# Kernel tuning notes

Measured on AMD Instinct MI355X. Metric: run time of the kernel, lower is better.

## Reference

```python
import jax, jax.numpy as jnp
import numpy as np

B, S, E, H = 4, 2048, 1024, 16
D = E // H
LR_MULT = 100.0
EPS = 1e-5

def setup_inputs() -> dict:
    key = jax.random.key(0)
    ks = jax.random.split(key, 4)
    x = jax.random.normal(ks[0], (B, S, E), dtype=jnp.float32)
    # nn.MultiheadAttention in_proj_weight [3E,E], out_proj.weight [E,E] (bias=False)
    W_qkv = jax.random.normal(ks[1], (3 * E, E), dtype=jnp.float32) * (1.0 / np.sqrt(E))
    W_o = jax.random.normal(ks[2], (E, E), dtype=jnp.float32) * (1.0 / np.sqrt(E))
    ln_w = jnp.ones((E,), dtype=jnp.float32)
    scaler = jnp.asarray(1.0 / LR_MULT, dtype=jnp.float32)
    return {"x": x, "W_qkv": W_qkv, "W_o": W_o, "ln_w": ln_w, "scaler": scaler}

def _layernorm(x, w):
    mu = jnp.mean(x, axis=-1, keepdims=True)
    var = jnp.mean(jnp.square(x - mu), axis=-1, keepdims=True)
    return (x - mu) * jax.lax.rsqrt(var + EPS) * w

def reference(x, W_qkv, W_o, ln_w, scaler):
    resid = x
    xn = _layernorm(x, ln_w)
    qkv = jnp.einsum('bse,fe->bsf', xn, W_qkv)  # [B,S,3E]
    q, k, v = jnp.split(qkv, 3, axis=-1)
    q = q.reshape(B, S, H, D)
    k = k.reshape(B, S, H, D)
    v = v.reshape(B, S, H, D)
    scores = jnp.einsum('bihd,bjhd->bhij', q, k) / jnp.sqrt(jnp.asarray(D, x.dtype))
    # linear_encoding_base[i,j] = j - i; bias = softplus(100*scaler)*(j-i) where j<=i else -inf
    i_idx = jnp.arange(S)
    rel = (i_idx[None, :] - i_idx[:, None]).astype(x.dtype)  # j - i
    causal = i_idx[None, :] <= i_idx[:, None]                # tril: j <= i
    slope = jax.nn.softplus(LR_MULT * scaler)
    bias = jnp.where(causal, slope * rel, -jnp.inf)          # [S,S]
    att = jax.nn.softmax(scores + bias[None, None, :, :], axis=-1)
    out = jnp.einsum('bhij,bjhd->bihd', att, v).reshape(B, S, E)
    out = jnp.einsum('bse,fe->bsf', out, W_o)
    return out + resid
```

## Files before the change

kernel.cpp:

```cpp
#include <hip/hip_runtime.h>

typedef unsigned short u16;
typedef unsigned int u32;
typedef __bf16 bf16x8 __attribute__((ext_vector_type(8)));
typedef float f32x4 __attribute__((ext_vector_type(4)));

#define B_ 4
#define S_ 2048
#define E_ 1024
#define H_ 16
#define D_ 64

__device__ __forceinline__ u16 f2bf(float f) {
  u32 u = __float_as_uint(f);
  u32 r = u + 0x7fffu + ((u >> 16) & 1u);
  return (u16)(r >> 16);
}

__device__ __forceinline__ void gload16(const u16* g, u16* l) {
  __builtin_amdgcn_global_load_lds((const __attribute__((address_space(1))) void*)g,
                                   (__attribute__((address_space(3))) void*)l, 16, 0, 0);
}

__global__ __launch_bounds__(256) void prep_kernel(const float* __restrict__ x,
                                                   const float* __restrict__ lnw,
                                                   u16* __restrict__ xn,
                                                   const float* __restrict__ Wqkv,
                                                   u16* __restrict__ wqkvb,
                                                   const float* __restrict__ Wo,
                                                   u16* __restrict__ wob) {
  const int b = blockIdx.x;
  if (b < 2048) {
    const int lane = threadIdx.x & 63;
    const int wv = threadIdx.x >> 6;
    const int row = b * 4 + wv;
    const float4* xr = (const float4*)(x + (size_t)row * E_);
    float4 vv[4];
    float s = 0.f, sq = 0.f;
#pragma unroll
    for (int i = 0; i < 4; ++i) {
      vv[i] = xr[lane + i * 64];
      s += vv[i].x + vv[i].y + vv[i].z + vv[i].w;
      sq += vv[i].x * vv[i].x + vv[i].y * vv[i].y + vv[i].z * vv[i].z + vv[i].w * vv[i].w;
    }
#pragma unroll
    for (int off = 1; off < 64; off <<= 1) {
      s += __shfl_xor(s, off);
      sq += __shfl_xor(sq, off);
    }
    const float mu = s * (1.f / E_);
    const float rs = rsqrtf(sq * (1.f / E_) - mu * mu + 1e-5f);
    u16* xo = xn + (size_t)row * E_;
    const float4* wr = (const float4*)lnw;
#pragma unroll
    for (int i = 0; i < 4; ++i) {
      float4 w4 = wr[lane + i * 64];
      ushort4 o;
      o.x = f2bf((vv[i].x - mu) * rs * w4.x);
      o.y = f2bf((vv[i].y - mu) * rs * w4.y);
      o.z = f2bf((vv[i].z - mu) * rs * w4.z);
      o.w = f2bf((vv[i].w - mu) * rs * w4.w);
      ((ushort4*)xo)[lane + i * 64] = o;
    }
  } else {
    const float* src = (b < 5120) ? Wqkv : Wo;
    u16* dst = (b < 5120) ? wqkvb : wob;
    const int i = (b < 5120 ? b - 2048 : b - 5120) * 256 + threadIdx.x;
    float4 v = ((const float4*)src)[i];
    ushort4 o;
    o.x = f2bf(v.x);
    o.y = f2bf(v.y);
    o.z = f2bf(v.z);
    o.w = f2bf(v.w);
    ((ushort4*)dst)[i] = o;
  }
}

__global__ __launch_bounds__(512, 2) void gemm8_qkv(const u16* __restrict__ A,
                                                    const u16* __restrict__ Bw,
                                                    u16* __restrict__ qo,
                                                    u16* __restrict__ ko,
                                                    u16* __restrict__ vo) {
  constexpr int K = 1024;
  constexpr int NT = K / 64;
  __shared__ u16 lds[2][2][256 * 64];
  const int t = threadIdx.x;
  const int lane = t & 63, wv = t >> 6;
  const int wm = wv >> 2, wn = wv & 3;
  const int m0 = blockIdx.y * 256, n0 = blockIdx.x * 256;
  const int r16 = lane & 15, g4 = lane >> 4;
  const int l3 = lane >> 3, l7 = lane & 7;
  const int colsrc = ((l7 ^ l3) * 8);

  f32x4 acc[8][4] = {};
  bf16x8 af[8][2];
  bf16x8 bfr[2][2];

  auto issue = [&](int ph, int buf, int kt) {
#pragma unroll
    for (int s = 0; s < 2; ++s) {
      const int j = wv * 2 + s;
      int c, m;
      if (ph == 0)      { m = 0; c = j + (j & 8); }
      else if (ph == 1) { m = 1; c = (j >> 2) * 8 + (j & 3); }
      else if (ph == 2) { m = 0; c = 8 + j + (j & 8); }
      else              { m = 1; c = (j >> 2) * 8 + 4 + (j & 3); }
      const u16* src = (m == 0 ? A + (size_t)(m0 + c * 8 + l3) * K
                               : Bw + (size_t)(n0 + c * 8 + l3) * K) + kt + colsrc;
      gload16(src, &lds[buf][m][c * 512]);
    }
  };

  auto loadA = [&](const u16* As, int half) {
#pragma unroll
    for (int i = 0; i < 4; ++i) {
      const int mi = half * 4 + i;
      const int r = wm * 128 + mi * 16 + r16;
      const int sw = (r & 7) << 3;
#pragma unroll
      for (int kc = 0; kc < 2; ++kc)
        af[mi][kc] = *(const bf16x8*)&As[r * 64 + ((kc * 32 + g4 * 8) ^ sw)];
    }
  };
  auto loadB = [&](const u16* Bs, int pair) {
#pragma unroll
    for (int n2 = 0; n2 < 2; ++n2) {
      const int r = wn * 64 + (pair * 2 + n2) * 16 + r16;
      const int sw = (r & 7) << 3;
#pragma unroll
      for (int kc = 0; kc < 2; ++kc)
        bfr[n2][kc] = *(const bf16x8*)&Bs[r * 64 + ((kc * 32 + g4 * 8) ^ sw)];
    }
  };
  auto mmac = [&](int mhalf, int npair) {
#pragma unroll
    for (int i = 0; i < 4; ++i)
#pragma unroll
      for (int n2 = 0; n2 < 2; ++n2)
#pragma unroll
        for (int kc = 0; kc < 2; ++kc)
          acc[mhalf * 4 + i][npair * 2 + n2] = __builtin_amdgcn_mfma_f32_16x16x32_bf16(
              af[mhalf * 4 + i][kc], bfr[n2][kc], acc[mhalf * 4 + i][npair * 2 + n2], 0, 0, 0);
  };

  issue(0, 0, 0);
  issue(1, 0, 0);
  issue(2, 0, 0);
  issue(3, 0, 0);
  asm volatile("s_waitcnt vmcnt(0)" ::: "memory");
  __builtin_amdgcn_s_barrier();

  for (int kt2 = 0; kt2 < NT - 1; ++kt2) {
    const int cur = kt2 & 1;
    const u16* As = lds[cur][0];
    const u16* Bs = lds[cur][1];
    const int ktN = (kt2 + 1) * 64;
    loadA(As, 0);
    loadB(Bs, 0);
    issue(0, cur ^ 1, ktN);
    issue(1, cur ^ 1, ktN);
    issue(2, cur ^ 1, ktN);
    issue(3, cur ^ 1, ktN);
    __builtin_amdgcn_s_barrier();
    asm volatile("s_waitcnt lgkmcnt(0)" ::: "memory");
    asm volatile("s_waitcnt vmcnt(10)" ::: "memory");
    __builtin_amdgcn_sched_barrier(0);
    __builtin_amdgcn_s_setprio(1);
    mmac(0, 0);
    __builtin_amdgcn_s_setprio(0);
    __builtin_amdgcn_s_barrier();
    loadA(As, 1);
    __builtin_amdgcn_s_barrier();
    asm volatile("s_waitcnt lgkmcnt(0)" ::: "memory");
    asm volatile("s_waitcnt vmcnt(8)" ::: "memory");
    __builtin_amdgcn_sched_barrier(0);
    __builtin_amdgcn_s_setprio(1);
    mmac(1, 0);
    __builtin_amdgcn_s_setprio(0);
    __builtin_amdgcn_s_barrier();
    loadB(Bs, 1);
    __builtin_amdgcn_s_barrier();
    asm volatile("s_waitcnt lgkmcnt(0)" ::: "memory");
    asm volatile("s_waitcnt vmcnt(4)" ::: "memory");
    __builtin_amdgcn_sched_barrier(0);
    __builtin_amdgcn_s_setprio(1);
    mmac(1, 1);
    mmac(0, 1);
    __builtin_amdgcn_s_setprio(0);
    __builtin_amdgcn_s_barrier();
  }
  {
    const int cur = (NT - 1) & 1;
    const u16* As = lds[cur][0];
    const u16* Bs = lds[cur][1];
    loadA(As, 0);
    loadB(Bs, 0);
    __builtin_amdgcn_s_barrier();
    asm volatile("s_waitcnt lgkmcnt(0)" ::: "memory");
    asm volatile("s_waitcnt vmcnt(2)" ::: "memory");
    __builtin_amdgcn_sched_barrier(0);
    __builtin_amdgcn_s_setprio(1);
    mmac(0, 0);
    __builtin_amdgcn_s_setprio(0);
    __builtin_amdgcn_s_barrier();
    loadA(As, 1);
    __builtin_amdgcn_s_barrier();
    asm volatile("s_waitcnt lgkmcnt(0)" ::: "memory");
    asm volatile("s_waitcnt vmcnt(0)" ::: "memory");
    __builtin_amdgcn_sched_barrier(0);
    __builtin_amdgcn_s_setprio(1);
    mmac(1, 0);
    __builtin_amdgcn_s_setprio(0);
    __builtin_amdgcn_s_barrier();
    loadB(Bs, 1);
    asm volatile("s_waitcnt lgkmcnt(0)" ::: "memory");
    __builtin_amdgcn_sched_barrier(0);
    __builtin_amdgcn_s_setprio(1);
    mmac(1, 1);
    mmac(0, 1);
    __builtin_amdgcn_s_setprio(0);
  }

  const int which = n0 >> 10;
  u16* dst = which == 0 ? qo : (which == 1 ? ko : vo);
#pragma unroll
  for (int mi = 0; mi < 8; ++mi)
#pragma unroll
    for (int e = 0; e < 4; ++e) {
      const int gr = m0 + wm * 128 + mi * 16 + g4 * 4 + e;
      const int bb = gr >> 11, ss = gr & 2047;
#pragma unroll
      for (int ni = 0; ni < 4; ++ni) {
        const int gc = n0 + wn * 64 + ni * 16 + r16;
        const int hh = (gc >> 6) & 15;
        const int dd = gc & 63;
        dst[(((size_t)bb * H_ + hh) * S_ + ss) * D_ + dd] = f2bf(acc[mi][ni][e]);
      }
    }
}

__global__ __launch_bounds__(256, 2) void gemm_bt1(const u16* __restrict__ A,
                                                   const u16* __restrict__ Bw,
                                                   const int K,
                                                   const float* __restrict__ xres,
                                                   float* __restrict__ outp) {
  __shared__ u16 lds[2][2][128 * 64];
  const int t = threadIdx.x;
  const int lane = t & 63, wv = t >> 6;
  const int wm = wv >> 1, wn = wv & 1;
  const int d = blockIdx.y * 8 + blockIdx.x;
  const int lin = (d & 7) * 64 + (d >> 3);
  const int m0 = (lin & 63) * 128, n0 = (lin >> 6) * 128;
  const int r16 = lane & 15, g4 = lane >> 4;

  const f32x4 fzero = {0.f, 0.f, 0.f, 0.f};
  f32x4 acc[4][4];
#pragma unroll
  for (int i = 0; i < 4; ++i)
#pragma unroll
    for (int j = 0; j < 4; ++j) acc[i][j] = fzero;

  const int srow8 = lane >> 3;
  const int scol = (lane & 7) * 8;

  auto stage = [&](int bu, int kt) {
#pragma unroll
    for (int i = 0; i < 4; ++i) {
      const int c = wv * 4 + i;
      const int row = c * 8 + srow8;
      gload16(A + (size_t)(m0 + row) * K + kt + scol, &lds[bu][0][c * 512]);
      gload16(Bw + (size_t)(n0 + row) * K + kt + scol, &lds[bu][1][c * 512]);
    }
  };

  auto compute = [&](int bu) {
    const u16* As = lds[bu][0];
    const u16* Bs = lds[bu][1];
    bf16x8 af[4][2], bfr[4][2];
#pragma unroll
    for (int mi = 0; mi < 4; ++mi)
#pragma unroll
      for (int kc = 0; kc < 2; ++kc)
        af[mi][kc] = *(const bf16x8*)&As[(wm * 64 + mi * 16 + r16) * 64 + kc * 32 + g4 * 8];
#pragma unroll
    for (int ni = 0; ni < 4; ++ni)
#pragma unroll
      for (int kc = 0; kc < 2; ++kc)
        bfr[ni][kc] = *(const bf16x8*)&Bs[(wn * 64 + ni * 16 + r16) * 64 + kc * 32 + g4 * 8];
#pragma unroll
    for (int mi = 0; mi < 4; ++mi)
#pragma unroll
      for (int ni = 0; ni < 4; ++ni)
#pragma unroll
        for (int kc = 0; kc < 2; ++kc)
          acc[mi][ni] = __builtin_amdgcn_mfma_f32_16x16x32_bf16(af[mi][kc], bfr[ni][kc],
                                                                acc[mi][ni], 0, 0, 0);
  };

  stage(0, 0);
  __syncthreads();
  int cur = 0;
  for (int kt = 64; kt < K; kt += 64) {
    stage(cur ^ 1, kt);
    compute(cur);
    __syncthreads();
    cur ^= 1;
  }
  compute(cur);

#pragma unroll
  for (int mi = 0; mi < 4; ++mi)
#pragma unroll
    for (int e = 0; e < 4; ++e) {
      const int gr = m0 + wm * 64 + mi * 16 + g4 * 4 + e;
#pragma unroll
      for (int ni = 0; ni < 4; ++ni) {
        const int gc = n0 + wn * 64 + ni * 16 + r16;
        const size_t idx = (size_t)gr * 1024 + gc;
        outp[idx] = acc[mi][ni][e] + xres[idx];
      }
    }
}

__global__ __launch_bounds__(256) void attn_kernel(const u16* __restrict__ q,
                                                   const u16* __restrict__ k,
                                                   const u16* __restrict__ v,
                                                   const float* __restrict__ scaler_p,
                                                   u16* __restrict__ ao) {
  __shared__ u16 Qs[64 * 72];
  __shared__ u16 Ks[64 * 72];
  __shared__ u16 Vt[64 * 72];
  __shared__ u16 Ps[4 * 16 * 72];
  const int t = threadIdx.x;
  const int lane = t & 63, wv = t >> 6;
  const int r16 = lane & 15, g4 = lane >> 4;
  const int it = blockIdx.x;
  const int bh = blockIdx.y;
  const int bb = bh >> 4, hh = bh & 15;
  const size_t base = (size_t)bh * (S_ * D_);

  const float tt = 100.f * scaler_p[0];
  const float slope = (tt > 20.f) ? tt : log1pf(expf(tt));
  const float L2E = 1.4426950408889634f;
  const float qs_l2e = 0.125f * L2E;
  const float sl_l2e = slope * L2E;
  int nb = (int)ceilf(80.f / (slope * 64.f));
  if (nb < 1) nb = 1;
  int jt0 = it - nb;
  if (jt0 < 0) jt0 = 0;

  {
    const int r = t >> 2, c = (t & 3) << 4;
    const u16* gp = q + base + (size_t)(it * 64 + r) * D_ + c;
    uint4 a0 = ((const uint4*)gp)[0];
    uint4 a1 = ((const uint4*)gp)[1];
    *(uint4*)&Qs[r * 72 + c] = a0;
    *(uint4*)&Qs[r * 72 + c + 8] = a1;
  }

  float mrun[4] = {-3e38f, -3e38f, -3e38f, -3e38f};
  float lrun[4] = {0.f, 0.f, 0.f, 0.f};
  const f32x4 fzero = {0.f, 0.f, 0.f, 0.f};
  f32x4 oacc[4];
#pragma unroll
  for (int i = 0; i < 4; ++i) oacc[i] = fzero;

  bf16x8 qa[2];
  bool qloaded = false;

  for (int jt = jt0; jt <= it; ++jt) {
    {
      const int r = t >> 2, c = (t & 3) << 4;
      const u16* kg = k + base + (size_t)(jt * 64 + r) * D_ + c;
      uint4 k0 = ((const uint4*)kg)[0];
      uint4 k1 = ((const uint4*)kg)[1];
      *(uint4*)&Ks[r * 72 + c] = k0;
      *(uint4*)&Ks[r * 72 + c + 8] = k1;
      const u16* vg = v + base + (size_t)(jt * 64 + r) * D_ + c;
      union { uint4 u; u16 s[8]; } v0, v1;
      v0.u = ((const uint4*)vg)[0];
      v1.u = ((const uint4*)vg)[1];
#pragma unroll
      for (int j = 0; j < 8; ++j) {
        Vt[(c + j) * 72 + r] = v0.s[j];
        Vt[(c + 8 + j) * 72 + r] = v1.s[j];
      }
    }
    __syncthreads();
    if (!qloaded) {
      qloaded = true;
#pragma unroll
      for (int kc = 0; kc < 2; ++kc)
        qa[kc] = *(const bf16x8*)&Qs[(wv * 16 + r16) * 72 + kc * 32 + g4 * 8];
    }
    f32x4 sfr[4];
#pragma unroll
    for (int nt = 0; nt < 4; ++nt) {
      sfr[nt] = fzero;
#pragma unroll
      for (int kc = 0; kc < 2; ++kc) {
        bf16x8 kb = *(const bf16x8*)&Ks[(nt * 16 + r16) * 72 + kc * 32 + g4 * 8];
        sfr[nt] = __builtin_amdgcn_mfma_f32_16x16x32_bf16(qa[kc], kb, sfr[nt], 0, 0, 0);
      }
    }
    const bool diag = (jt == it);
    const float jb = (float)((jt - it) * 64);
    float pm[4] = {-3e38f, -3e38f, -3e38f, -3e38f};
#pragma unroll
    for (int nt = 0; nt < 4; ++nt) {
      const int jl = nt * 16 + r16;
#pragma unroll
      for (int e = 0; e < 4; ++e) {
        const int il = wv * 16 + g4 * 4 + e;
        float sc = sfr[nt][e] * qs_l2e + sl_l2e * (jb + (float)(jl - il));
        if (diag && jl > il) sc = -3e38f;
        sfr[nt][e] = sc;
        pm[e] = fmaxf(pm[e], sc);
      }
    }
#pragma unroll
    for (int e = 0; e < 4; ++e) {
#pragma unroll
      for (int off = 1; off < 16; off <<= 1) pm[e] = fmaxf(pm[e], __shfl_xor(pm[e], off));
    }
    u16* Psw = Ps + wv * (16 * 72);
    float psum[4] = {0.f, 0.f, 0.f, 0.f};
#pragma unroll
    for (int e = 0; e < 4; ++e) {
      const float mn = fmaxf(mrun[e], pm[e]);
      const float rsc = exp2f(mrun[e] - mn);
      mrun[e] = mn;
      lrun[e] *= rsc;
#pragma unroll
      for (int nt = 0; nt < 4; ++nt) oacc[nt][e] *= rsc;
    }
#pragma unroll
    for (int nt = 0; nt < 4; ++nt)
#pragma unroll
      for (int e = 0; e < 4; ++e) {
        const float p = exp2f(sfr[nt][e] - mrun[e]);
        psum[e] += p;
        Psw[(g4 * 4 + e) * 72 + nt * 16 + r16] = f2bf(p);
      }
#pragma unroll
    for (int e = 0; e < 4; ++e) {
#pragma unroll
      for (int off = 1; off < 16; off <<= 1) psum[e] += __shfl_xor(psum[e], off);
      lrun[e] += psum[e];
    }
    bf16x8 pa[2];
#pragma unroll
    for (int jk = 0; jk < 2; ++jk)
      pa[jk] = *(const bf16x8*)&Psw[r16 * 72 + jk * 32 + g4 * 8];
#pragma unroll
    for (int nt = 0; nt < 4; ++nt)
#pragma unroll
      for (int jk = 0; jk < 2; ++jk) {
        bf16x8 vb = *(const bf16x8*)&Vt[(nt * 16 + r16) * 72 + jk * 32 + g4 * 8];
        oacc[nt] = __builtin_amdgcn_mfma_f32_16x16x32_bf16(pa[jk], vb, oacc[nt], 0, 0, 0);
      }
    __syncthreads();
  }
#pragma unroll
  for (int e = 0; e < 4; ++e) {
    const float inv = 1.f / lrun[e];
    const int row = it * 64 + wv * 16 + g4 * 4 + e;
#pragma unroll
    for (int nt = 0; nt < 4; ++nt) {
      const int col = hh * 64 + nt * 16 + r16;
      ao[((size_t)bb * S_ + row) * E_ + col] = f2bf(oacc[nt][e] * inv);
    }
  }
}

extern "C" void kernel_launch(void* const* d_in, const int* in_sizes, int n_in,
                              void* d_out, int out_size, void* d_ws, size_t ws_size,
                              hipStream_t stream) {
  const float* x = (const float*)d_in[0];
  const float* Wqkv = (const float*)d_in[1];
  const float* Wo = (const float*)d_in[2];
  const float* lnw = (const float*)d_in[3];
  const float* scaler = (const float*)d_in[4];
  float* out = (float*)d_out;
  char* ws = (char*)d_ws;

  u16* xn = (u16*)(ws + 0);
  u16* q = (u16*)(ws + 16777216);
  u16* kk = (u16*)(ws + 33554432);
  u16* vv = (u16*)(ws + 50331648);
  u16* ao = (u16*)(ws + 67108864);
  u16* wqkvb = (u16*)(ws + 83886080);
  u16* wob = (u16*)(ws + 90177536);

  prep_kernel<<<6144, 256, 0, stream>>>(x, lnw, xn, Wqkv, wqkvb, Wo, wob);
  gemm8_qkv<<<dim3(12, 32), 512, 0, stream>>>(xn, wqkvb, q, kk, vv);
  attn_kernel<<<dim3(32, 64), 256, 0, stream>>>(q, kk, vv, scaler, ao);
  gemm_bt1<<<dim3(8, 64), 256, 0, stream>>>(ao, wob, 1024, x, out);
}
```

Before: 139.4 us.

## Single-buffer QKV GEMM LDS with phased in-place refills to raise occupancy

Halves the QKV GEMM's shared memory by replacing the double-buffered LDS tiles with one buffer. Each phase of the next k-tile is loaded in place once the registers have read the data it overwrites. Launch bounds go from 2 to 4 blocks per CU to exploit the freed LDS and hide latency with more resident waves. The cost is a tighter cross-wave dependency, since writes can only start after everyone has finished reading that region. Register pressure may also rise, because the 128-entry accumulator must fit the tighter occupancy bound.

```diff
diff --git a/kernel.cpp b/kernel.cpp
--- a/kernel.cpp
+++ b/kernel.cpp
@@ -76,14 +76,14 @@
   }
 }
 
-__global__ __launch_bounds__(512, 2) void gemm8_qkv(const u16* __restrict__ A,
+__global__ __launch_bounds__(512, 4) void gemm8_qkv(const u16* __restrict__ A,
                                                     const u16* __restrict__ Bw,
                                                     u16* __restrict__ qo,
                                                     u16* __restrict__ ko,
                                                     u16* __restrict__ vo) {
   constexpr int K = 1024;
   constexpr int NT = K / 64;
-  __shared__ u16 lds[2][2][256 * 64];
+  __shared__ u16 lds[2][256 * 64];
   const int t = threadIdx.x;
   const int lane = t & 63, wv = t >> 6;
   const int wm = wv >> 2, wn = wv & 3;
@@ -96,7 +96,7 @@
   bf16x8 af[8][2];
   bf16x8 bfr[2][2];
 
-  auto issue = [&](int ph, int buf, int kt) {
+  auto issue = [&](int ph, int kt) {
 #pragma unroll
     for (int s = 0; s < 2; ++s) {
       const int j = wv * 2 + s;
@@ -107,11 +107,12 @@
       else              { m = 1; c = (j >> 2) * 8 + 4 + (j & 3); }
       const u16* src = (m == 0 ? A + (size_t)(m0 + c * 8 + l3) * K
                                : Bw + (size_t)(n0 + c * 8 + l3) * K) + kt + colsrc;
-      gload16(src, &lds[buf][m][c * 512]);
-    }
-  };
-
-  auto loadA = [&](const u16* As, int half) {
+      gload16(src, &lds[m][c * 512]);
+    }
+  };
+
+  auto loadA = [&](int half) {
+    const u16* As = lds[0];
 #pragma unroll
     for (int i = 0; i < 4; ++i) {
       const int mi = half * 4 + i;
@@ -122,7 +123,8 @@
         af[mi][kc] = *(const bf16x8*)&As[r * 64 + ((kc * 32 + g4 * 8) ^ sw)];
     }
   };
-  auto loadB = [&](const u16* Bs, int pair) {
+  auto loadB = [&](int pair) {
+    const u16* Bs = lds[1];
 #pragma unroll
     for (int n2 = 0; n2 < 2; ++n2) {
       const int r = wn * 64 + (pair * 2 + n2) * 16 + r16;
@@ -143,68 +145,66 @@
               af[mhalf * 4 + i][kc], bfr[n2][kc], acc[mhalf * 4 + i][npair * 2 + n2], 0, 0, 0);
   };
 
-  issue(0, 0, 0);
-  issue(1, 0, 0);
-  issue(2, 0, 0);
-  issue(3, 0, 0);
+  issue(0, 0);
+  issue(1, 0);
+  issue(2, 0);
+  issue(3, 0);
   asm volatile("s_waitcnt vmcnt(0)" ::: "memory");
   __builtin_amdgcn_s_barrier();
 
   for (int kt2 = 0; kt2 < NT - 1; ++kt2) {
-    const int cur = kt2 & 1;
-    const u16* As = lds[cur][0];
-    const u16* Bs = lds[cur][1];
     const int ktN = (kt2 + 1) * 64;
-    loadA(As, 0);
-    loadB(Bs, 0);
-    issue(0, cur ^ 1, ktN);
-    issue(1, cur ^ 1, ktN);
-    issue(2, cur ^ 1, ktN);
-    issue(3, cur ^ 1, ktN);
-    __builtin_amdgcn_s_barrier();
-    asm volatile("s_waitcnt lgkmcnt(0)" ::: "memory");
-    asm volatile("s_waitcnt vmcnt(10)" ::: "memory");
+    loadA(0);
+    loadB(0);
+    asm volatile("s_waitcnt lgkmcnt(0)" ::: "memory");
+    __builtin_amdgcn_sched_barrier(0);
+    __builtin_amdgcn_s_barrier();
+    issue(0, ktN);
+    issue(1, ktN);
+    asm volatile("s_waitcnt vmcnt(6)" ::: "memory");
     __builtin_amdgcn_sched_barrier(0);
     __builtin_amdgcn_s_setprio(1);
     mmac(0, 0);
     __builtin_amdgcn_s_setprio(0);
     __builtin_amdgcn_s_barrier();
-    loadA(As, 1);
-    __builtin_amdgcn_s_barrier();
-    asm volatile("s_waitcnt lgkmcnt(0)" ::: "memory");
-    asm volatile("s_waitcnt vmcnt(8)" ::: "memory");
+    loadA(1);
+    asm volatile("s_waitcnt lgkmcnt(0)" ::: "memory");
+    __builtin_amdgcn_sched_barrier(0);
+    __builtin_amdgcn_s_barrier();
+    issue(2, ktN);
+    asm volatile("s_waitcnt vmcnt(6)" ::: "memory");
     __builtin_amdgcn_sched_barrier(0);
     __builtin_amdgcn_s_setprio(1);
     mmac(1, 0);
     __builtin_amdgcn_s_setprio(0);
     __builtin_amdgcn_s_barrier();
-    loadB(Bs, 1);
-    __builtin_amdgcn_s_barrier();
-    asm volatile("s_waitcnt lgkmcnt(0)" ::: "memory");
+    loadB(1);
+    asm volatile("s_waitcnt lgkmcnt(0)" ::: "memory");
+    __builtin_amdgcn_sched_barrier(0);
+    __builtin_amdgcn_s_barrier();
+    issue(3, ktN);
     asm volatile("s_waitcnt vmcnt(4)" ::: "memory");
     __builtin_amdgcn_sched_barrier(0);
     __builtin_amdgcn_s_setprio(1);
     mmac(1, 1);
+    __builtin_amdgcn_s_setprio(0);
+    __builtin_amdgcn_s_barrier();
+    __builtin_amdgcn_s_setprio(1);
     mmac(0, 1);
     __builtin_amdgcn_s_setprio(0);
-    __builtin_amdgcn_s_barrier();
   }
   {
-    const int cur = (NT - 1) & 1;
-    const u16* As = lds[cur][0];
-    const u16* Bs = lds[cur][1];
-    loadA(As, 0);
-    loadB(Bs, 0);
-    __builtin_amdgcn_s_barrier();
-    asm volatile("s_waitcnt lgkmcnt(0)" ::: "memory");
+    loadA(0);
+    loadB(0);
+    asm volatile("s_waitcnt lgkmcnt(0)" ::: "memory");
+    __builtin_amdgcn_sched_barrier(0);
     asm volatile("s_waitcnt vmcnt(2)" ::: "memory");
     __builtin_amdgcn_sched_barrier(0);
     __builtin_amdgcn_s_setprio(1);
     mmac(0, 0);
     __builtin_amdgcn_s_setprio(0);
     __builtin_amdgcn_s_barrier();
-    loadA(As, 1);
-    __builtin_amdgcn_s_barrier();
+    loadA(1);
     asm volatile("s_waitcnt lgkmcnt(0)" ::: "memory");
     asm volatile("s_waitcnt vmcnt(0)" ::: "memory");
     __builtin_amdgcn_sched_barrier(0);
@@ -212,7 +212,7 @@
     mmac(1, 0);
     __builtin_amdgcn_s_setprio(0);
     __builtin_amdgcn_s_barrier();
-    loadB(Bs, 1);
+    loadB(1);
     asm volatile("s_waitcnt lgkmcnt(0)" ::: "memory");
     __builtin_amdgcn_sched_barrier(0);
     __builtin_amdgcn_s_setprio(1);
```

Result: slower. 533.8 us (+282.9%).
